# Kernel tuning notes

Measured on AMD Instinct MI355X. Metric: run time of the kernel, lower is better.

## Reference

```python
import jax, jax.numpy as jnp
import numpy as np

N_PTS = 2_000_000
N_VOX = 500_000
N_EMB = 1_000_000
EMBED_DIM = 16


def _interp_offset():
    # 8 corners of the unit cube, same order as torch.meshgrid([0,1]*3) -> reshape(-1,3)
    o = jnp.array([0.0, 1.0], dtype=jnp.float32)
    return jnp.stack(jnp.meshgrid(o, o, o, indexing='ij'), axis=-1).reshape(-1, 3)  # [8,3]


def setup_inputs() -> dict:
    key = jax.random.key(0)
    k1, k2, k3, k4, k5 = jax.random.split(key, 5)
    pts = jax.random.uniform(k1, (N_PTS, 3), dtype=jnp.float32)
    p2v_idx = jax.random.randint(k2, (N_PTS,), 0, N_VOX, dtype=jnp.int64 if jax.config.jax_enable_x64 else jnp.int32)
    embeddings = jax.random.normal(k3, (N_EMB, EMBED_DIM), dtype=jnp.float32) * (EMBED_DIM ** -0.5)
    center_points = jax.random.uniform(k4, (N_VOX, 3), dtype=jnp.float32)
    center2corner = jax.random.randint(k5, (N_VOX, 8), 0, N_EMB, dtype=jnp.int64 if jax.config.jax_enable_x64 else jnp.int32)
    voxel_size = jnp.ones((1,), dtype=jnp.float32)
    return {"pts": pts, "p2v_idx": p2v_idx, "embeddings": embeddings,
            "center_points": center_points, "center2corner": center2corner,
            "voxel_size": voxel_size}


def reference(pts, p2v_idx, embeddings, center_points, center2corner, voxel_size):
    offset = _interp_offset()                      # [8,3]
    cp = center_points[p2v_idx]                    # [N,3]   gather voxel centers
    cidx = center2corner[p2v_idx]                  # [N,8]   gather corner indices
    emb = embeddings[cidx]                         # [N,8,D] gather corner embeddings
    # relative position inside voxel, in [0,1]
    p = (pts - cp) / voxel_size + 0.5              # [N,3]
    p = p[:, None, :]                              # [N,1,3]
    # trilinear weights: prod over xyz of (p if corner==1 else 1-p)
    r = jnp.prod(p * offset + (1.0 - p) * (1.0 - offset), axis=-1)  # [N,8]
    return jnp.einsum('nc,ncd->nd', r, emb)        # [N,D]
```

## Files before the change

kernel.cpp:

```cpp
#include <hip/hip_runtime.h>


typedef float v4f __attribute__((ext_vector_type(4)));

__global__ void k_zero(unsigned* __restrict__ hist, int n) {
    int i = blockIdx.x * blockDim.x + threadIdx.x;
    if (i < n) hist[i] = 0u;
}

__global__ void k_hist_rank(const int* __restrict__ p2v,
                            unsigned* __restrict__ hist,
                            unsigned* __restrict__ rank, int N) {
    int i = blockIdx.x * blockDim.x + threadIdx.x;
    if (i < N) rank[i] = atomicAdd(&hist[p2v[i]], 1u);
}

__global__ __launch_bounds__(256) void k_scan_blocks(unsigned* __restrict__ hist,
                                                     unsigned* __restrict__ bsums, int nbins) {
    __shared__ unsigned tsum[256];
    const int tid = threadIdx.x;
    const int i0 = blockIdx.x * 1024 + tid * 4;
    unsigned v[4]; unsigned s = 0;
    #pragma unroll
    for (int k = 0; k < 4; ++k) {
        unsigned c = (i0 + k < nbins) ? hist[i0 + k] : 0u;
        v[k] = s; s += c;
    }
    tsum[tid] = s; __syncthreads();
    for (int off = 1; off < 256; off <<= 1) {
        unsigned x = tsum[tid];
        unsigned y = (tid >= off) ? tsum[tid - off] : 0u;
        __syncthreads();
        tsum[tid] = x + y;
        __syncthreads();
    }
    unsigned prefix = (tid > 0) ? tsum[tid - 1] : 0u;
    #pragma unroll
    for (int k = 0; k < 4; ++k) {
        if (i0 + k < nbins) hist[i0 + k] = prefix + v[k];
    }
    if (tid == 255) bsums[blockIdx.x] = tsum[255];
}

__global__ __launch_bounds__(256) void k_scan_sums(unsigned* __restrict__ bsums, int nb) {
    __shared__ unsigned tsum[256];
    const int tid = threadIdx.x;
    const int i0 = tid * 4;
    unsigned v[4]; unsigned s = 0;
    #pragma unroll
    for (int k = 0; k < 4; ++k) {
        unsigned c = (i0 + k < nb) ? bsums[i0 + k] : 0u;
        v[k] = s; s += c;
    }
    tsum[tid] = s; __syncthreads();
    for (int off = 1; off < 256; off <<= 1) {
        unsigned x = tsum[tid];
        unsigned y = (tid >= off) ? tsum[tid - off] : 0u;
        __syncthreads();
        tsum[tid] = x + y;
        __syncthreads();
    }
    unsigned prefix = (tid > 0) ? tsum[tid - 1] : 0u;
    #pragma unroll
    for (int k = 0; k < 4; ++k) {
        if (i0 + k < nb) bsums[i0 + k] = prefix + v[k];
    }
}

__global__ void k_add(unsigned* __restrict__ hist, const unsigned* __restrict__ bsums, int nbins) {
    int i = blockIdx.x * blockDim.x + threadIdx.x;
    if (i < nbins) hist[i] += bsums[i >> 10];
}

__global__ __launch_bounds__(256) void k_place(
    const float* __restrict__ pts,
    const int*   __restrict__ p2v,
    const unsigned* __restrict__ rank,
    const unsigned* __restrict__ hist,
    unsigned* __restrict__ vsort,
    v4f*      __restrict__ rec,
    int N)
{
    int i = blockIdx.x * blockDim.x + threadIdx.x;
    if (i >= N) return;
    const int v = p2v[i];
    const unsigned pos = hist[v] + rank[i];
    vsort[pos] = (unsigned)v;
    v4f r;
    r.x = pts[3 * (size_t)i + 0];
    r.y = pts[3 * (size_t)i + 1];
    r.z = pts[3 * (size_t)i + 2];
    r.w = __int_as_float(i);
    rec[pos] = r;
}

__global__ __launch_bounds__(256) void k_main(
    const unsigned* __restrict__ vsort, const v4f* __restrict__ rec,
    const float* __restrict__ emb,
    const float* __restrict__ cp,
    const int*   __restrict__ c2c,
    const float* __restrict__ vox,
    float*       __restrict__ out,
    int N)
{
    const int t = blockIdx.x * blockDim.x + threadIdx.x;
    const int n = t >> 2;
    const int q = t & 3;
    if (n >= N) return;

    const unsigned v = vsort[n];
    const v4f r = rec[n];
    const int orig = __float_as_int(r.w);

    const int4* c4 = (const int4*)(c2c + 8 * (size_t)v);
    const int4 ci0 = c4[0];
    const int4 ci1 = c4[1];
    const int cidx[8] = {ci0.x, ci0.y, ci0.z, ci0.w, ci1.x, ci1.y, ci1.z, ci1.w};

    v4f e[8];
    #pragma unroll
    for (int c = 0; c < 8; ++c) {
        e[c] = *(const v4f*)(emb + 16 * (size_t)cidx[c] + 4 * q);
    }

    const float inv_vs = 1.0f / vox[0];
    const float* cpp = cp + 3 * (size_t)v;
    const float px = (r.x - cpp[0]) * inv_vs + 0.5f;
    const float py = (r.y - cpp[1]) * inv_vs + 0.5f;
    const float pz = (r.z - cpp[2]) * inv_vs + 0.5f;
    const float wx[2] = {1.0f - px, px};
    const float wy[2] = {1.0f - py, py};
    const float wz[2] = {1.0f - pz, pz};

    v4f acc = (v4f)(0.0f);
    #pragma unroll
    for (int c = 0; c < 8; ++c) {
        const float w = wx[(c >> 2) & 1] * wy[(c >> 1) & 1] * wz[c & 1];
        acc.x = fmaf(w, e[c].x, acc.x);
        acc.y = fmaf(w, e[c].y, acc.y);
        acc.z = fmaf(w, e[c].z, acc.z);
        acc.w = fmaf(w, e[c].w, acc.w);
    }

    __builtin_nontemporal_store(acc, (v4f*)(out + 16 * (size_t)orig + 4 * q));
}

__global__ __launch_bounds__(256) void k_direct(
    const float* __restrict__ pts, const int* __restrict__ p2v,
    const float* __restrict__ emb, const float* __restrict__ cp,
    const int* __restrict__ c2c, const float* __restrict__ vox,
    float* __restrict__ out, int N)
{
    const int t = blockIdx.x * blockDim.x + threadIdx.x;
    const int n = t >> 2, q = t & 3;
    if (n >= N) return;
    const int v = p2v[n];
    const int4* c4 = (const int4*)(c2c + 8 * (size_t)v);
    const int4 ci0 = c4[0], ci1 = c4[1];
    const int cidx[8] = {ci0.x, ci0.y, ci0.z, ci0.w, ci1.x, ci1.y, ci1.z, ci1.w};
    v4f e[8];
    #pragma unroll
    for (int c = 0; c < 8; ++c) e[c] = *(const v4f*)(emb + 16 * (size_t)cidx[c] + 4 * q);
    const float inv_vs = 1.0f / vox[0];
    const float* pp = pts + 3 * (size_t)n;
    const float* cpp = cp + 3 * (size_t)v;
    const float px = (pp[0] - cpp[0]) * inv_vs + 0.5f;
    const float py = (pp[1] - cpp[1]) * inv_vs + 0.5f;
    const float pz = (pp[2] - cpp[2]) * inv_vs + 0.5f;
    const float wx[2] = {1.0f - px, px};
    const float wy[2] = {1.0f - py, py};
    const float wz[2] = {1.0f - pz, pz};
    v4f acc = (v4f)(0.0f);
    #pragma unroll
    for (int c = 0; c < 8; ++c) {
        const float w = wx[(c >> 2) & 1] * wy[(c >> 1) & 1] * wz[c & 1];
        acc.x = fmaf(w, e[c].x, acc.x); acc.y = fmaf(w, e[c].y, acc.y);
        acc.z = fmaf(w, e[c].z, acc.z); acc.w = fmaf(w, e[c].w, acc.w);
    }
    __builtin_nontemporal_store(acc, (v4f*)(out + 4 * (size_t)t));
}

extern "C" void kernel_launch(void* const* d_in, const int* in_sizes, int n_in,
                              void* d_out, int out_size, void* d_ws, size_t ws_size,
                              hipStream_t stream) {
    const float* pts = (const float*)d_in[0];
    const int*   p2v = (const int*)d_in[1];
    const float* emb = (const float*)d_in[2];
    const float* cp  = (const float*)d_in[3];
    const int*   c2c = (const int*)d_in[4];
    const float* vox = (const float*)d_in[5];
    float*       out = (float*)d_out;

    const int N  = in_sizes[1];
    const int NV = in_sizes[4] / 8;

    const size_t off_hist  = 0;
    const size_t off_bsums = 2u * 1024u * 1024u;
    const size_t off_rank  = 4u * 1024u * 1024u;
    const size_t off_vsort = 12u * 1024u * 1024u;
    const size_t off_rec   = 20u * 1024u * 1024u;
    const size_t need = off_rec + (size_t)N * 16u;

    if (ws_size < need) {
        const int block = 256;
        const long long threads = 4LL * N;
        k_direct<<<(int)((threads + block - 1) / block), block, 0, stream>>>(
            pts, p2v, emb, cp, c2c, vox, out, N);
        return;
    }

    unsigned* hist  = (unsigned*)((char*)d_ws + off_hist);
    unsigned* bsums = (unsigned*)((char*)d_ws + off_bsums);
    unsigned* rank  = (unsigned*)((char*)d_ws + off_rank);
    unsigned* vsort = (unsigned*)((char*)d_ws + off_vsort);
    v4f*      rec   = (v4f*)((char*)d_ws + off_rec);

    const int block = 256;
    const int nscan = (NV + 1023) / 1024;

    k_zero<<<(NV + block - 1) / block, block, 0, stream>>>(hist, NV);
    k_hist_rank<<<(N + block - 1) / block, block, 0, stream>>>(p2v, hist, rank, N);
    k_scan_blocks<<<nscan, 256, 0, stream>>>(hist, bsums, NV);
    k_scan_sums<<<1, 256, 0, stream>>>(bsums, nscan);
    k_add<<<(NV + block - 1) / block, block, 0, stream>>>(hist, bsums, NV);
    k_place<<<(N + block - 1) / block, block, 0, stream>>>(pts, p2v, rank, hist, vsort, rec, N);

    const long long threads = 4LL * N;
    k_main<<<(int)((threads + block - 1) / block), block, 0, stream>>>(
        vsort, rec, emb, cp, c2c, vox, out, N);
}
```

Measured before the change: 478.0 us.

## Fold scan block offsets into placement and vectorize histogram and placement kernels

Removes the k_add kernel by having k_place add the block-level prefix from bsums directly when computing each point's position. The histogram-rank and placement kernels now handle 8 and 4 points per thread, using int4/uint4/float4 loads and stores for p2v, rank and pts. This saves one launch and one pass over the histogram, and batches memory transactions. In exchange it adds an extra gather into bsums per point and cuts the thread count, which may lower latency hiding for the random atomics and scatters.

```diff
diff --git a/kernel.cpp b/kernel.cpp
--- a/kernel.cpp
+++ b/kernel.cpp
@@ -8,11 +8,29 @@
     if (i < n) hist[i] = 0u;
 }
 
-__global__ void k_hist_rank(const int* __restrict__ p2v,
-                            unsigned* __restrict__ hist,
-                            unsigned* __restrict__ rank, int N) {
-    int i = blockIdx.x * blockDim.x + threadIdx.x;
-    if (i < N) rank[i] = atomicAdd(&hist[p2v[i]], 1u);
+__global__ __launch_bounds__(256) void k_hist_rank(const int* __restrict__ p2v,
+                                                   unsigned* __restrict__ hist,
+                                                   unsigned* __restrict__ rank, int N) {
+    const int base = (blockIdx.x * blockDim.x + threadIdx.x) * 8;
+    if (base + 7 < N) {
+        const int4 a = *(const int4*)(p2v + base);
+        const int4 b = *(const int4*)(p2v + base + 4);
+        const unsigned r0 = atomicAdd(&hist[a.x], 1u);
+        const unsigned r1 = atomicAdd(&hist[a.y], 1u);
+        const unsigned r2 = atomicAdd(&hist[a.z], 1u);
+        const unsigned r3 = atomicAdd(&hist[a.w], 1u);
+        const unsigned r4 = atomicAdd(&hist[b.x], 1u);
+        const unsigned r5 = atomicAdd(&hist[b.y], 1u);
+        const unsigned r6 = atomicAdd(&hist[b.z], 1u);
+        const unsigned r7 = atomicAdd(&hist[b.w], 1u);
+        uint4 o0; o0.x = r0; o0.y = r1; o0.z = r2; o0.w = r3;
+        uint4 o1; o1.x = r4; o1.y = r5; o1.z = r6; o1.w = r7;
+        *(uint4*)(rank + base)     = o0;
+        *(uint4*)(rank + base + 4) = o1;
+    } else {
+        for (int k = 0; k < 8; ++k)
+            if (base + k < N) rank[base + k] = atomicAdd(&hist[p2v[base + k]], 1u);
+    }
 }
 
 __global__ __launch_bounds__(256) void k_scan_blocks(unsigned* __restrict__ hist,
@@ -67,31 +85,60 @@
     }
 }
 
-__global__ void k_add(unsigned* __restrict__ hist, const unsigned* __restrict__ bsums, int nbins) {
-    int i = blockIdx.x * blockDim.x + threadIdx.x;
-    if (i < nbins) hist[i] += bsums[i >> 10];
-}
-
 __global__ __launch_bounds__(256) void k_place(
     const float* __restrict__ pts,
     const int*   __restrict__ p2v,
     const unsigned* __restrict__ rank,
     const unsigned* __restrict__ hist,
+    const unsigned* __restrict__ bsums,
     unsigned* __restrict__ vsort,
     v4f*      __restrict__ rec,
     int N)
 {
-    int i = blockIdx.x * blockDim.x + threadIdx.x;
-    if (i >= N) return;
-    const int v = p2v[i];
-    const unsigned pos = hist[v] + rank[i];
-    vsort[pos] = (unsigned)v;
-    v4f r;
-    r.x = pts[3 * (size_t)i + 0];
-    r.y = pts[3 * (size_t)i + 1];
-    r.z = pts[3 * (size_t)i + 2];
-    r.w = __int_as_float(i);
-    rec[pos] = r;
+    const int base = (blockIdx.x * blockDim.x + threadIdx.x) * 4;
+    if (base + 3 < N) {
+        const int4  v4r = *(const int4*)(p2v + base);
+        const uint4 r4  = *(const uint4*)(rank + base);
+        const v4f* p4 = (const v4f*)pts;
+        const size_t f0i = (size_t)(3 * (base >> 2));
+        const v4f f0 = p4[f0i];
+        const v4f f1 = p4[f0i + 1];
+        const v4f f2 = p4[f0i + 2];
+
+        const unsigned pos0 = hist[v4r.x] + bsums[((unsigned)v4r.x) >> 10] + r4.x;
+        const unsigned pos1 = hist[v4r.y] + bsums[((unsigned)v4r.y) >> 10] + r4.y;
+        const unsigned pos2 = hist[v4r.z] + bsums[((unsigned)v4r.z) >> 10] + r4.z;
+        const unsigned pos3 = hist[v4r.w] + bsums[((unsigned)v4r.w) >> 10] + r4.w;
+
+        vsort[pos0] = (unsigned)v4r.x;
+        vsort[pos1] = (unsigned)v4r.y;
+        vsort[pos2] = (unsigned)v4r.z;
+        vsort[pos3] = (unsigned)v4r.w;
+
+        v4f a;
+        a.x = f0.x; a.y = f0.y; a.z = f0.z; a.w = __int_as_float(base + 0);
+        rec[pos0] = a;
+        a.x = f0.w; a.y = f1.x; a.z = f1.y; a.w = __int_as_float(base + 1);
+        rec[pos1] = a;
+        a.x = f1.z; a.y = f1.w; a.z = f2.x; a.w = __int_as_float(base + 2);
+        rec[pos2] = a;
+        a.x = f2.y; a.y = f2.z; a.z = f2.w; a.w = __int_as_float(base + 3);
+        rec[pos3] = a;
+    } else {
+        for (int k = 0; k < 4; ++k) {
+            const int i = base + k;
+            if (i >= N) break;
+            const int v = p2v[i];
+            const unsigned pos = hist[v] + bsums[((unsigned)v) >> 10] + rank[i];
+            vsort[pos] = (unsigned)v;
+            v4f r;
+            r.x = pts[3 * (size_t)i + 0];
+            r.y = pts[3 * (size_t)i + 1];
+            r.z = pts[3 * (size_t)i + 2];
+            r.w = __int_as_float(i);
+            rec[pos] = r;
+        }
+    }
 }
 
 __global__ __launch_bounds__(256) void k_main(
@@ -219,11 +266,11 @@
     const int nscan = (NV + 1023) / 1024;
 
     k_zero<<<(NV + block - 1) / block, block, 0, stream>>>(hist, NV);
-    k_hist_rank<<<(N + block - 1) / block, block, 0, stream>>>(p2v, hist, rank, N);
+    k_hist_rank<<<(N + block * 8 - 1) / (block * 8), block, 0, stream>>>(p2v, hist, rank, N);
     k_scan_blocks<<<nscan, 256, 0, stream>>>(hist, bsums, NV);
     k_scan_sums<<<1, 256, 0, stream>>>(bsums, nscan);
-    k_add<<<(NV + block - 1) / block, block, 0, stream>>>(hist, bsums, NV);
-    k_place<<<(N + block - 1) / block, block, 0, stream>>>(pts, p2v, rank, hist, vsort, rec, N);
+    k_place<<<(N + block * 4 - 1) / (block * 4), block, 0, stream>>>(
+        pts, p2v, rank, hist, bsums, vsort, rec, N);
 
     const long long threads = 4LL * N;
     k_main<<<(int)((threads + block - 1) / block), block, 0, stream>>>(
```

New measurement: 458.5 us. -4.1%, faster.
